# Kernel tuning notes

Hardware: AMD Instinct MI355X
Metric: run time of the kernel (lower is better)

Reference implementation:

```python
import jax, jax.numpy as jnp
import numpy as np

N = 50000   # nodes
E = 800000  # edges
B = 64      # graphs in batch
IN = 128    # in_features
HID = 64    # hidden_channels
H = 4       # head_count
C = 10      # out_classes
NEG = 0.2   # leaky relu negative slope
EPS = 1e-5  # batchnorm eps (eval mode, running mean 0 / var 1)


def _gat(x, edge_index, W, a_src, a_dst, b):
    """PyG GATConv (add_self_loops=False, concat=True), eval mode (no dropout)."""
    Hh, F = a_src.shape
    xW = (x @ W).reshape(-1, Hh, F)                       # [N,H,F]
    src, dst = edge_index[0], edge_index[1]
    e = (jnp.einsum('nhf,hf->nh', xW, a_src)[src]
         + jnp.einsum('nhf,hf->nh', xW, a_dst)[dst])      # [E,H]
    e = jnp.where(e > 0, e, NEG * e)                      # leaky relu
    m = jax.ops.segment_max(e, dst, num_segments=N)       # per-dst max
    m = jnp.where(jnp.isfinite(m), m, 0.0)
    p = jnp.exp(e - m[dst])
    denom = jax.ops.segment_sum(p, dst, num_segments=N)
    alpha = p / jnp.maximum(denom[dst], 1e-16)            # edge softmax over dst
    out = jax.ops.segment_sum(alpha[:, :, None] * xW[src], dst, num_segments=N)
    return out.reshape(-1, Hh * F) + b


def _bn_relu(y, g, be):
    # BatchNorm1d in eval mode with running_mean=0, running_var=1, then ReLU
    return jax.nn.relu(g * y / jnp.sqrt(1.0 + EPS) + be)


def setup_inputs():
    key = jax.random.key(0)
    ks = jax.random.split(key, 24)
    s = lambda k, shape: (jax.random.normal(k, shape, jnp.float32) * 0.05)
    z = lambda shape: jnp.zeros(shape, jnp.float32)
    o = lambda shape: jnp.ones(shape, jnp.float32)
    return {
        'acc_flag': 0,
        'x': jax.random.normal(ks[0], (N, IN), jnp.float32),
        'edge_index': jax.random.randint(ks[1], (2, E), 0, N),
        'batch': jnp.sort(jax.random.randint(ks[2], (N,), 0, B)),
        # layer 1: GATConv(IN -> HID, heads=H, concat)
        'W1': s(ks[3], (IN, H * HID)), 'a_src1': s(ks[4], (H, HID)), 'a_dst1': s(ks[5], (H, HID)), 'b1': z((H * HID,)),
        # proj: GATConv(H*HID -> HID, heads=1) + BN
        'W2': s(ks[6], (H * HID, HID)), 'a_src2': s(ks[7], (1, HID)), 'a_dst2': s(ks[8], (1, HID)), 'b2': z((HID,)), 'g2': o((HID,)), 'be2': z((HID,)),
        # block 1
        'W3': s(ks[9], (HID, HID)), 'a_src3': s(ks[10], (1, HID)), 'a_dst3': s(ks[11], (1, HID)), 'b3': z((HID,)), 'g3': o((HID,)), 'be3': z((HID,)),
        # block 2
        'W4': s(ks[12], (HID, HID)), 'a_src4': s(ks[13], (1, HID)), 'a_dst4': s(ks[14], (1, HID)), 'b4': z((HID,)), 'g4': o((HID,)), 'be4': z((HID,)),
        # MLP head
        'Wh1': s(ks[15], (HID, 128)), 'bh1': z((128,)),
        'Wh2': s(ks[16], (128, C)), 'bh2': z((C,)),
    }


def reference(acc_flag, x, edge_index, batch,
              W1, a_src1, a_dst1, b1,
              W2, a_src2, a_dst2, b2, g2, be2,
              W3, a_src3, a_dst3, b3, g3, be3,
              W4, a_src4, a_dst4, b4, g4, be4,
              Wh1, bh1, Wh2, bh2):
    # hardware GAT layer + ReLU (relu applied twice in original -> idempotent)
    x1 = jax.nn.relu(_gat(x, edge_index, W1, a_src1, a_dst1, b1))   # [N, H*HID]
    # projection block: residual base is zeros (shape mismatch H*HID vs HID)
    h = _bn_relu(_gat(x1, edge_index, W2, a_src2, a_dst2, b2), g2, be2)
    # residual blocks (shapes match -> x + relu(bn(y)))
    h = h + _bn_relu(_gat(h, edge_index, W3, a_src3, a_dst3, b3), g3, be3)
    h = h + _bn_relu(_gat(h, edge_index, W4, a_src4, a_dst4, b4), g4, be4)
    # global mean pool over graphs
    pooled = jax.ops.segment_sum(h, batch, num_segments=B)
    cnt = jnp.maximum(jax.ops.segment_sum(jnp.ones((N,), h.dtype), batch, num_segments=B), 1.0)
    hp = pooled / cnt[:, None]                                      # [B, HID]
    # MLP head
    return jax.nn.relu(hp @ Wh1 + bh1) @ Wh2 + bh2                  # [B, C]
```

## Files before the change

kernel.cpp:

```cpp
#include <hip/hip_runtime.h>

#define N_NODES 50000
#define N_EDGES 800000
#define N_GRAPHS 64
#define NEG_SLOPE 0.2f
#define BN_RSQ 0.9999950000374997f
#define NB_SCAN ((N_NODES + 255) / 256)

typedef __bf16 bf16x8 __attribute__((ext_vector_type(8)));
typedef float floatx4 __attribute__((ext_vector_type(4)));

__device__ __forceinline__ float lrelu(float v) { return v > 0.0f ? v : NEG_SLOPE * v; }

__device__ __forceinline__ float b2f(unsigned short u) {
    return __uint_as_float(((unsigned int)u) << 16);
}
__device__ __forceinline__ unsigned short f2b(float f) {
    unsigned int u = __float_as_uint(f);
    return (unsigned short)((u + 0x7fffu + ((u >> 16) & 1u)) >> 16);
}
__device__ __forceinline__ float blo(unsigned int d) { return __uint_as_float(d << 16); }
__device__ __forceinline__ float bhi(unsigned int d) { return __uint_as_float(d & 0xffff0000u); }

__global__ void k_prep(const int* __restrict__ ei, int* __restrict__ deg,
                       const float* __restrict__ W1, const float* __restrict__ W2,
                       const float* __restrict__ W3, const float* __restrict__ W4,
                       unsigned short* __restrict__ Wt1, unsigned short* __restrict__ Wt2,
                       unsigned short* __restrict__ Wt3, unsigned short* __restrict__ Wt4) {
    int i = blockIdx.x * 256 + threadIdx.x;
    if (i < 32768) {
        int k = i >> 8, n = i & 255;
        Wt1[n * 128 + k] = f2b(W1[i]);
    } else if (i < 49152) {
        int j = i - 32768;
        int k = j >> 6, n = j & 63;
        Wt2[n * 256 + k] = f2b(W2[j]);
    } else if (i < 53248) {
        int j = i - 49152;
        int k = j >> 6, n = j & 63;
        Wt3[n * 64 + k] = f2b(W3[j]);
    } else if (i < 57344) {
        int j = i - 53248;
        int k = j >> 6, n = j & 63;
        Wt4[n * 64 + k] = f2b(W4[j]);
    }
    if (i < N_EDGES) atomicAdd(&deg[ei[N_EDGES + i]], 1);
}

__global__ __launch_bounds__(256) void k_offs(const int* __restrict__ deg, int* __restrict__ offs,
                                              int* __restrict__ total, const int* __restrict__ batch,
                                              int* __restrict__ bounds, int* __restrict__ bh) {
    __shared__ int lh[64];
    if (threadIdx.x < 64) lh[threadIdx.x] = 0;
    __syncthreads();
    if (blockIdx.x == 0 && threadIdx.x <= N_GRAPHS) {
        int g = threadIdx.x;
        int lo = 0, hi = N_NODES;
        while (lo < hi) {
            int mid = (lo + hi) >> 1;
            if (batch[mid] < g) lo = mid + 1; else hi = mid;
        }
        bounds[g] = lo;
    }
    int i = blockIdx.x * blockDim.x + threadIdx.x;
    int lane = threadIdx.x & 63;
    int v = (i < N_NODES) ? deg[i] : 0;
    int incl = v;
    for (int o = 1; o < 64; o <<= 1) {
        int t = __shfl_up(incl, o);
        if (lane >= o) incl += t;
    }
    int wtot = __shfl(incl, 63);
    int base = 0;
    if (lane == 0) base = atomicAdd(total, wtot);
    base = __shfl(base, 0);
    if (i < N_NODES) {
        offs[i] = base + incl - v;
        atomicAdd(&lh[63 - min(v, 63)], 1);
    }
    __syncthreads();
    if (threadIdx.x < 64) bh[blockIdx.x * 64 + threadIdx.x] = lh[threadIdx.x];
}

__global__ __launch_bounds__(256) void k_pscan(const int* __restrict__ bh, int* __restrict__ bb) {
    __shared__ int partial[4][64];
    __shared__ int bbase[64];
    const int tid = threadIdx.x;
    const int b = tid & 63, q = tid >> 6;
    const int per = (NB_SCAN + 3) / 4;
    const int k0 = q * per, k1 = min(k0 + per, NB_SCAN);
    int s = 0;
    for (int k = k0; k < k1; ++k) s += bh[k * 64 + b];
    partial[q][b] = s;
    __syncthreads();
    if (tid < 64) {
        int tot = partial[0][tid] + partial[1][tid] + partial[2][tid] + partial[3][tid];
        int incl = tot;
        for (int o = 1; o < 64; o <<= 1) {
            int t2 = __shfl_up(incl, o);
            if (tid >= o) incl += t2;
        }
        bbase[tid] = incl - tot;
    }
    __syncthreads();
    int run = bbase[b];
    for (int q2 = 0; q2 < q; ++q2) run += partial[q2][b];
    for (int k = k0; k < k1; ++k) {
        bb[k * 64 + b] = run;
        run += bh[k * 64 + b];
    }
}

__global__ __launch_bounds__(256) void k_fillperm(const int* __restrict__ ei,
                                                  const int* __restrict__ offs,
                                                  int* __restrict__ cur, int* __restrict__ csr_src,
                                                  const int* __restrict__ deg,
                                                  const int* __restrict__ bb,
                                                  int* __restrict__ perm) {
    __shared__ int lcnt[64];
    if (blockIdx.x < NB_SCAN) {
        if (threadIdx.x < 64) lcnt[threadIdx.x] = 0;
        __syncthreads();
        int i = blockIdx.x * 256 + threadIdx.x;
        if (i < N_NODES) {
            int b = 63 - min(deg[i], 63);
            int r = atomicAdd(&lcnt[b], 1);
            perm[bb[blockIdx.x * 64 + b] + r] = i;
        }
    }
    int e = blockIdx.x * 256 + threadIdx.x;
    if (e < N_EDGES) {
        int d = ei[N_EDGES + e];
        int pos = offs[d] + atomicAdd(&cur[d], 1);
        csr_src[pos] = ei[e];
    }
}

template <int K, int N, int HEADS, bool AF32>
__global__ __launch_bounds__(256) void k_mgemm(const void* __restrict__ Ap,
                                               const unsigned short* __restrict__ Bt,
                                               const float* __restrict__ asrc,
                                               const float* __restrict__ adst,
                                               unsigned short* __restrict__ out,
                                               float* __restrict__ es,
                                               float* __restrict__ ed, int rows) {
    constexpr int LDP = K + 8;
    __shared__ unsigned short As[64 * LDP];
    const int tid = threadIdx.x;
    const int r0 = blockIdx.x * 64;
    if (AF32) {
        const float* A = (const float*)Ap;
        for (int i = tid; i < 16 * K; i += 256) {
            int r = i / (K / 4), c4 = i % (K / 4);
            int row = r0 + r;
            float4 v = (row < rows) ? *(const float4*)&A[(size_t)row * K + c4 * 4]
                                    : make_float4(0.f, 0.f, 0.f, 0.f);
            ushort4 u;
            u.x = f2b(v.x); u.y = f2b(v.y); u.z = f2b(v.z); u.w = f2b(v.w);
            *(ushort4*)&As[r * LDP + c4 * 4] = u;
        }
    } else {
        const unsigned short* A = (const unsigned short*)Ap;
        for (int i = tid; i < 8 * K; i += 256) {
            int r = i / (K / 8), c8 = i % (K / 8);
            int row = r0 + r;
            uint4 v;
            if (row < rows) v = *(const uint4*)&A[(size_t)row * K + c8 * 8];
            else { v.x = v.y = v.z = v.w = 0; }
            *(uint4*)&As[r * LDP + c8 * 8] = v;
        }
    }
    __syncthreads();
    const int w = tid >> 6, lane = tid & 63;
    const int quad = lane >> 4, l16 = lane & 15;
    const int gr0 = r0 + w * 16 + quad * 4;
    bf16x8 afrag[K / 32];
#pragma unroll
    for (int kk = 0; kk < K / 32; ++kk)
        afrag[kk] = *(const bf16x8*)&As[(w * 16 + l16) * LDP + kk * 32 + quad * 8];
    float sacc[4] = {0.f, 0.f, 0.f, 0.f};
    float dacc[4] = {0.f, 0.f, 0.f, 0.f};
#pragma unroll 1
    for (int ct = 0; ct < N / 16; ++ct) {
        floatx4 acc = {0.f, 0.f, 0.f, 0.f};
#pragma unroll
        for (int kk = 0; kk < K / 32; ++kk) {
            const bf16x8 bfrag =
                *(const bf16x8*)&Bt[(size_t)(ct * 16 + l16) * K + kk * 32 + quad * 8];
            acc = __builtin_amdgcn_mfma_f32_16x16x32_bf16(afrag[kk], bfrag, acc, 0, 0, 0);
        }
        const int gc = ct * 16 + l16;
        const int hh = gc >> 6;
        const int f = gc & 63;
        const float as = asrc[hh * 64 + f];
        const float ad = adst[hh * 64 + f];
#pragma unroll
        for (int rg = 0; rg < 4; ++rg) {
            sacc[rg] = fmaf(acc[rg], as, sacc[rg]);
            dacc[rg] = fmaf(acc[rg], ad, dacc[rg]);
        }
#pragma unroll
        for (int rg = 0; rg < 4; ++rg) {
            int gr = gr0 + rg;
            if (gr < rows) out[(size_t)gr * N + gc] = f2b(acc[rg]);
        }
        if ((ct & 3) == 3) {
#pragma unroll
            for (int rg = 0; rg < 4; ++rg) {
                float s = sacc[rg], d = dacc[rg];
                for (int o = 1; o < 16; o <<= 1) {
                    s += __shfl_xor(s, o);
                    d += __shfl_xor(d, o);
                }
                if (l16 == 0) {
                    int gr = gr0 + rg;
                    if (gr < rows) {
                        es[(size_t)gr * HEADS + hh] = s;
                        ed[(size_t)gr * HEADS + hh] = d;
                    }
                }
                sacc[rg] = 0.f;
                dacc[rg] = 0.f;
            }
        }
    }
}

__global__ __launch_bounds__(256) void k_gat1f(
    const unsigned short* __restrict__ xW, const float* __restrict__ es, const float* __restrict__ ed,
    const int* __restrict__ offs, const int* __restrict__ deg, const int* __restrict__ csr,
    const int* __restrict__ perm, const float* __restrict__ bias,
    const unsigned short* __restrict__ Bt2, const float* __restrict__ as2,
    const float* __restrict__ ad2, unsigned short* __restrict__ outW,
    float* __restrict__ es2o, float* __restrict__ ed2o) {
    __shared__ float ps[4][4 * 68];
    __shared__ int sbuf[4][64];
    __shared__ unsigned short As2[16 * 264];
    __shared__ int nbuf[16];
    __shared__ float sds[4][16], sdd[4][16];
    const int wv = threadIdx.x >> 6;
    const int lane = threadIdx.x & 63;
    const int grp = lane >> 4, t = lane & 15;
    const int h = t >> 2;
    const int r = wv * 4 + grp;
    const int pidx = blockIdx.x * 16 + r;
    const int n = perm[pidx];
    const int off = offs[n];
    const int dg = deg[n];
    const float4 edv = *(const float4*)&ed[n * 4];
    const int cb = t * 16;

    float acc[16];
#pragma unroll
    for (int k = 0; k < 16; ++k) acc[k] = 0.f;
    float dsum = 0.f;

    for (int base = 0; base < dg; base += 16) {
        const int idx = base + t;
        int s_l = 0;
        float p0 = 0.f, p1 = 0.f, p2 = 0.f, p3 = 0.f;
        if (idx < dg) {
            s_l = csr[off + idx];
            const float4 ev = *(const float4*)&es[s_l * 4];
            p0 = __expf(lrelu(ev.x + edv.x));
            p1 = __expf(lrelu(ev.y + edv.y));
            p2 = __expf(lrelu(ev.z + edv.z));
            p3 = __expf(lrelu(ev.w + edv.w));
        }
        *(float4*)&ps[wv][grp * 68 + t * 4] = make_float4(p0, p1, p2, p3);
        sbuf[wv][grp * 16 + t] = s_l;
        const int cnt = min(16, dg - base);
        const int cntR = (cnt + 3) & ~3;
        for (int j = 0; j < cntR; j += 4) {
            const float pa = ps[wv][grp * 68 + (j + 0) * 4 + h];
            const float pb = ps[wv][grp * 68 + (j + 1) * 4 + h];
            const float pc = ps[wv][grp * 68 + (j + 2) * 4 + h];
            const float pd = ps[wv][grp * 68 + (j + 3) * 4 + h];
            const int sa = sbuf[wv][grp * 16 + j + 0];
            const int sb = sbuf[wv][grp * 16 + j + 1];
            const int sc = sbuf[wv][grp * 16 + j + 2];
            const int sd = sbuf[wv][grp * 16 + j + 3];
            const uint4 a0 = *(const uint4*)&xW[(size_t)sa * 256 + cb];
            const uint4 a1 = *(const uint4*)&xW[(size_t)sa * 256 + cb + 8];
            const uint4 b0 = *(const uint4*)&xW[(size_t)sb * 256 + cb];
            const uint4 b1 = *(const uint4*)&xW[(size_t)sb * 256 + cb + 8];
            const uint4 c0 = *(const uint4*)&xW[(size_t)sc * 256 + cb];
            const uint4 c1 = *(const uint4*)&xW[(size_t)sc * 256 + cb + 8];
            const uint4 d0 = *(const uint4*)&xW[(size_t)sd * 256 + cb];
            const uint4 d1 = *(const uint4*)&xW[(size_t)sd * 256 + cb + 8];
            dsum += (pa + pb) + (pc + pd);
            acc[0]  = fmaf(pa, blo(a0.x), acc[0]);
            acc[1]  = fmaf(pa, bhi(a0.x), acc[1]);
            acc[2]  = fmaf(pa, blo(a0.y), acc[2]);
            acc[3]  = fmaf(pa, bhi(a0.y), acc[3]);
            acc[4]  = fmaf(pa, blo(a0.z), acc[4]);
            acc[5]  = fmaf(pa, bhi(a0.z), acc[5]);
            acc[6]  = fmaf(pa, blo(a0.w), acc[6]);
            acc[7]  = fmaf(pa, bhi(a0.w), acc[7]);
            acc[8]  = fmaf(pa, blo(a1.x), acc[8]);
            acc[9]  = fmaf(pa, bhi(a1.x), acc[9]);
            acc[10] = fmaf(pa, blo(a1.y), acc[10]);
            acc[11] = fmaf(pa, bhi(a1.y), acc[11]);
            acc[12] = fmaf(pa, blo(a1.z), acc[12]);
            acc[13] = fmaf(pa, bhi(a1.z), acc[13]);
            acc[14] = fmaf(pa, blo(a1.w), acc[14]);
            acc[15] = fmaf(pa, bhi(a1.w), acc[15]);
            acc[0]  = fmaf(pb, blo(b0.x), acc[0]);
            acc[1]  = fmaf(pb, bhi(b0.x), acc[1]);
            acc[2]  = fmaf(pb, blo(b0.y), acc[2]);
            acc[3]  = fmaf(pb, bhi(b0.y), acc[3]);
            acc[4]  = fmaf(pb, blo(b0.z), acc[4]);
            acc[5]  = fmaf(pb, bhi(b0.z), acc[5]);
            acc[6]  = fmaf(pb, blo(b0.w), acc[6]);
            acc[7]  = fmaf(pb, bhi(b0.w), acc[7]);
            acc[8]  = fmaf(pb, blo(b1.x), acc[8]);
            acc[9]  = fmaf(pb, bhi(b1.x), acc[9]);
            acc[10] = fmaf(pb, blo(b1.y), acc[10]);
            acc[11] = fmaf(pb, bhi(b1.y), acc[11]);
            acc[12] = fmaf(pb, blo(b1.z), acc[12]);
            acc[13] = fmaf(pb, bhi(b1.z), acc[13]);
            acc[14] = fmaf(pb, blo(b1.w), acc[14]);
            acc[15] = fmaf(pb, bhi(b1.w), acc[15]);
            acc[0]  = fmaf(pc, blo(c0.x), acc[0]);
            acc[1]  = fmaf(pc, bhi(c0.x), acc[1]);
            acc[2]  = fmaf(pc, blo(c0.y), acc[2]);
            acc[3]  = fmaf(pc, bhi(c0.y), acc[3]);
            acc[4]  = fmaf(pc, blo(c0.z), acc[4]);
            acc[5]  = fmaf(pc, bhi(c0.z), acc[5]);
            acc[6]  = fmaf(pc, blo(c0.w), acc[6]);
            acc[7]  = fmaf(pc, bhi(c0.w), acc[7]);
            acc[8]  = fmaf(pc, blo(c1.x), acc[8]);
            acc[9]  = fmaf(pc, bhi(c1.x), acc[9]);
            acc[10] = fmaf(pc, blo(c1.y), acc[10]);
            acc[11] = fmaf(pc, bhi(c1.y), acc[11]);
            acc[12] = fmaf(pc, blo(c1.z), acc[12]);
            acc[13] = fmaf(pc, bhi(c1.z), acc[13]);
            acc[14] = fmaf(pc, blo(c1.w), acc[14]);
            acc[15] = fmaf(pc, bhi(c1.w), acc[15]);
            acc[0]  = fmaf(pd, blo(d0.x), acc[0]);
            acc[1]  = fmaf(pd, bhi(d0.x), acc[1]);
            acc[2]  = fmaf(pd, blo(d0.y), acc[2]);
            acc[3]  = fmaf(pd, bhi(d0.y), acc[3]);
            acc[4]  = fmaf(pd, blo(d0.z), acc[4]);
            acc[5]  = fmaf(pd, bhi(d0.z), acc[5]);
            acc[6]  = fmaf(pd, blo(d0.w), acc[6]);
            acc[7]  = fmaf(pd, bhi(d0.w), acc[7]);
            acc[8]  = fmaf(pd, blo(d1.x), acc[8]);
            acc[9]  = fmaf(pd, bhi(d1.x), acc[9]);
            acc[10] = fmaf(pd, blo(d1.y), acc[10]);
            acc[11] = fmaf(pd, bhi(d1.y), acc[11]);
            acc[12] = fmaf(pd, blo(d1.z), acc[12]);
            acc[13] = fmaf(pd, bhi(d1.z), acc[13]);
            acc[14] = fmaf(pd, blo(d1.w), acc[14]);
            acc[15] = fmaf(pd, bhi(d1.w), acc[15]);
        }
    }
    const float inv = 1.0f / fmaxf(dsum, 1e-16f);
#pragma unroll
    for (int k4 = 0; k4 < 16; k4 += 4) {
        const int c = cb + k4;
        const float4 bv = *(const float4*)&bias[c];
        ushort4 o4;
        o4.x = f2b(fmaxf(fmaf(acc[k4 + 0], inv, bv.x), 0.f));
        o4.y = f2b(fmaxf(fmaf(acc[k4 + 1], inv, bv.y), 0.f));
        o4.z = f2b(fmaxf(fmaf(acc[k4 + 2], inv, bv.z), 0.f));
        o4.w = f2b(fmaxf(fmaf(acc[k4 + 3], inv, bv.w), 0.f));
        *(ushort4*)&As2[r * 264 + c] = o4;
    }
    if (t == 0) nbuf[r] = n;
    __syncthreads();

    {
        const int gc = wv * 16 + t;
        floatx4 c2 = {0.f, 0.f, 0.f, 0.f};
#pragma unroll
        for (int kk = 0; kk < 8; ++kk) {
            const bf16x8 af = *(const bf16x8*)&As2[t * 264 + kk * 32 + grp * 8];
            const bf16x8 bf = *(const bf16x8*)&Bt2[(size_t)gc * 256 + kk * 32 + grp * 8];
            c2 = __builtin_amdgcn_mfma_f32_16x16x32_bf16(af, bf, c2, 0, 0, 0);
        }
        const float a_s = as2[gc];
        const float a_d = ad2[gc];
        float srg[4], drg[4];
#pragma unroll
        for (int rg = 0; rg < 4; ++rg) {
            srg[rg] = c2[rg] * a_s;
            drg[rg] = c2[rg] * a_d;
            const int row = grp * 4 + rg;
            outW[(size_t)nbuf[row] * 64 + gc] = f2b(c2[rg]);
        }
#pragma unroll
        for (int rg = 0; rg < 4; ++rg) {
            for (int o = 1; o < 16; o <<= 1) {
                srg[rg] += __shfl_xor(srg[rg], o);
                drg[rg] += __shfl_xor(drg[rg], o);
            }
        }
        if (t == 0) {
#pragma unroll
            for (int rg = 0; rg < 4; ++rg) {
                sds[wv][grp * 4 + rg] = srg[rg];
                sdd[wv][grp * 4 + rg] = drg[rg];
            }
        }
    }
    __syncthreads();
    if (threadIdx.x < 16) {
        const int rr = threadIdx.x;
        es2o[nbuf[rr]] = sds[0][rr] + sds[1][rr] + sds[2][rr] + sds[3][rr];
        ed2o[nbuf[rr]] = sdd[0][rr] + sdd[1][rr] + sdd[2][rr] + sdd[3][rr];
    }
}

template <bool RES>
__global__ __launch_bounds__(256) void k_gatLG(
    const unsigned short* __restrict__ xW, const float* __restrict__ es, const float* __restrict__ ed,
    const int* __restrict__ offs, const int* __restrict__ deg, const int* __restrict__ csr,
    const int* __restrict__ perm, const float* __restrict__ bias, const float* __restrict__ gam,
    const float* __restrict__ bet, float* __restrict__ hglob,
    const unsigned short* __restrict__ Btn, const float* __restrict__ asn,
    const float* __restrict__ adn, unsigned short* __restrict__ outW,
    float* __restrict__ esn, float* __restrict__ edn_o) {
    __shared__ float ps[4][64];
    __shared__ int sbuf[4][64];
    __shared__ unsigned short As2[32 * 72];
    __shared__ int nbuf[32];
    __shared__ float sds[2][32], sdd[2][32];
    const int wv = threadIdx.x >> 6;
    const int lane = threadIdx.x & 63;
    const int g8 = lane >> 3, t8 = lane & 7;
    const int row1 = wv * 8 + g8;
    const int pbase = blockIdx.x * 32;
    const int pidx = pbase + row1;
    const bool valid = pidx < N_NODES;
    const int n = perm[valid ? pidx : 0];
    const int off = offs[n];
    const int dg = valid ? deg[n] : 0;
    const float edn = valid ? ed[n] : 0.f;
    const int cb = t8 * 8;

    float acc[8];
#pragma unroll
    for (int k = 0; k < 8; ++k) acc[k] = 0.f;
    float dsum = 0.f;

    for (int base = 0; base < dg; base += 8) {
        const int idx = base + t8;
        int s_l = 0;
        float p_l = 0.f;
        if (idx < dg) {
            s_l = csr[off + idx];
            p_l = __expf(lrelu(es[s_l] + edn));
        }
        ps[wv][g8 * 8 + t8] = p_l;
        sbuf[wv][g8 * 8 + t8] = s_l;
        float pp[8];
        int ss[8];
#pragma unroll
        for (int q = 0; q < 8; ++q) {
            pp[q] = ps[wv][g8 * 8 + q];
            ss[q] = sbuf[wv][g8 * 8 + q];
        }
        uint4 u[8];
#pragma unroll
        for (int q = 0; q < 8; ++q) u[q] = *(const uint4*)&xW[(size_t)ss[q] * 64 + cb];
#pragma unroll
        for (int q = 0; q < 8; ++q) {
            dsum += pp[q];
            acc[0] = fmaf(pp[q], blo(u[q].x), acc[0]);
            acc[1] = fmaf(pp[q], bhi(u[q].x), acc[1]);
            acc[2] = fmaf(pp[q], blo(u[q].y), acc[2]);
            acc[3] = fmaf(pp[q], bhi(u[q].y), acc[3]);
            acc[4] = fmaf(pp[q], blo(u[q].z), acc[4]);
            acc[5] = fmaf(pp[q], bhi(u[q].z), acc[5]);
            acc[6] = fmaf(pp[q], blo(u[q].w), acc[6]);
            acc[7] = fmaf(pp[q], bhi(u[q].w), acc[7]);
        }
    }
    const float inv = 1.0f / fmaxf(dsum, 1e-16f);
    float hn[8];
#pragma unroll
    for (int k = 0; k < 8; ++k) {
        const int c = cb + k;
        const float y = fmaf(acc[k], inv, bias[c]);
        const float z = fmaxf(fmaf(gam[c] * y, BN_RSQ, bet[c]), 0.f);
        hn[k] = (RES && valid) ? hglob[(size_t)n * 64 + c] + z : z;
    }
    if (valid) {
        *(float4*)&hglob[(size_t)n * 64 + cb] = make_float4(hn[0], hn[1], hn[2], hn[3]);
        *(float4*)&hglob[(size_t)n * 64 + cb + 4] = make_float4(hn[4], hn[5], hn[6], hn[7]);
    }
    ushort4 u0, u1;
    u0.x = f2b(hn[0]); u0.y = f2b(hn[1]); u0.z = f2b(hn[2]); u0.w = f2b(hn[3]);
    u1.x = f2b(hn[4]); u1.y = f2b(hn[5]); u1.z = f2b(hn[6]); u1.w = f2b(hn[7]);
    if (!valid) { u0.x = u0.y = u0.z = u0.w = 0; u1.x = u1.y = u1.z = u1.w = 0; }
    *(ushort4*)&As2[row1 * 72 + cb] = u0;
    *(ushort4*)&As2[row1 * 72 + cb + 4] = u1;
    if (t8 == 0) nbuf[row1] = n;
    __syncthreads();

    {
        const int quad = lane >> 4, l16 = lane & 15;
        const int rs = wv >> 1;
        float sacc[4] = {0.f, 0.f, 0.f, 0.f};
        float dacc[4] = {0.f, 0.f, 0.f, 0.f};
#pragma unroll
        for (int ci = 0; ci < 2; ++ci) {
            const int ct = (wv & 1) * 2 + ci;
            const int gc = ct * 16 + l16;
            floatx4 c2 = {0.f, 0.f, 0.f, 0.f};
#pragma unroll
            for (int kk = 0; kk < 2; ++kk) {
                const bf16x8 af = *(const bf16x8*)&As2[(rs * 16 + l16) * 72 + kk * 32 + quad * 8];
                const bf16x8 bf = *(const bf16x8*)&Btn[(size_t)gc * 64 + kk * 32 + quad * 8];
                c2 = __builtin_amdgcn_mfma_f32_16x16x32_bf16(af, bf, c2, 0, 0, 0);
            }
            const float a_s = asn[gc];
            const float a_d = adn[gc];
#pragma unroll
            for (int rg = 0; rg < 4; ++rg) {
                sacc[rg] = fmaf(c2[rg], a_s, sacc[rg]);
                dacc[rg] = fmaf(c2[rg], a_d, dacc[rg]);
                const int row = rs * 16 + quad * 4 + rg;
                if (pbase + row < N_NODES) outW[(size_t)nbuf[row] * 64 + gc] = f2b(c2[rg]);
            }
        }
#pragma unroll
        for (int rg = 0; rg < 4; ++rg) {
            for (int o = 1; o < 16; o <<= 1) {
                sacc[rg] += __shfl_xor(sacc[rg], o);
                dacc[rg] += __shfl_xor(dacc[rg], o);
            }
        }
        if (l16 == 0) {
#pragma unroll
            for (int rg = 0; rg < 4; ++rg) {
                sds[wv & 1][rs * 16 + quad * 4 + rg] = sacc[rg];
                sdd[wv & 1][rs * 16 + quad * 4 + rg] = dacc[rg];
            }
        }
    }
    __syncthreads();
    if (threadIdx.x < 32) {
        const int rr = threadIdx.x;
        if (pbase + rr < N_NODES) {
            esn[nbuf[rr]] = sds[0][rr] + sds[1][rr];
            edn_o[nbuf[rr]] = sdd[0][rr] + sdd[1][rr];
        }
    }
}

__global__ __launch_bounds__(256) void k_gatF(
    const unsigned short* __restrict__ xW, const float* __restrict__ es, const float* __restrict__ ed,
    const int* __restrict__ offs, const int* __restrict__ deg, const int* __restrict__ csr,
    const int* __restrict__ perm, const float* __restrict__ bias, const float* __restrict__ gam,
    const float* __restrict__ bet, float* __restrict__ h) {
    __shared__ float ps[4][64];
    __shared__ int sbuf[4][64];
    const int wv = threadIdx.x >> 6;
    const int lane = threadIdx.x & 63;
    const int grp = lane >> 3, t = lane & 7;
    const int pidx = blockIdx.x * 32 + wv * 8 + grp;
    if (pidx >= N_NODES) return;
    const int n = perm[pidx];
    const int off = offs[n];
    const int dg = deg[n];
    const float edn = ed[n];
    const int cb = t * 8;

    float acc[8];
#pragma unroll
    for (int k = 0; k < 8; ++k) acc[k] = 0.f;
    float dsum = 0.f;

    for (int base = 0; base < dg; base += 8) {
        const int idx = base + t;
        int s_l = 0;
        float p_l = 0.f;
        if (idx < dg) {
            s_l = csr[off + idx];
            p_l = __expf(lrelu(es[s_l] + edn));
        }
        ps[wv][grp * 8 + t] = p_l;
        sbuf[wv][grp * 8 + t] = s_l;
        float pp[8];
        int ss[8];
#pragma unroll
        for (int q = 0; q < 8; ++q) {
            pp[q] = ps[wv][grp * 8 + q];
            ss[q] = sbuf[wv][grp * 8 + q];
        }
        uint4 u[8];
#pragma unroll
        for (int q = 0; q < 8; ++q) u[q] = *(const uint4*)&xW[(size_t)ss[q] * 64 + cb];
#pragma unroll
        for (int q = 0; q < 8; ++q) {
            dsum += pp[q];
            acc[0] = fmaf(pp[q], blo(u[q].x), acc[0]);
            acc[1] = fmaf(pp[q], bhi(u[q].x), acc[1]);
            acc[2] = fmaf(pp[q], blo(u[q].y), acc[2]);
            acc[3] = fmaf(pp[q], bhi(u[q].y), acc[3]);
            acc[4] = fmaf(pp[q], blo(u[q].z), acc[4]);
            acc[5] = fmaf(pp[q], bhi(u[q].z), acc[5]);
            acc[6] = fmaf(pp[q], blo(u[q].w), acc[6]);
            acc[7] = fmaf(pp[q], bhi(u[q].w), acc[7]);
        }
    }
    const float inv = 1.0f / fmaxf(dsum, 1e-16f);
    float hn[8];
#pragma unroll
    for (int k = 0; k < 8; ++k) {
        const int c = cb + k;
        const float y = fmaf(acc[k], inv, bias[c]);
        const float z = fmaxf(fmaf(gam[c] * y, BN_RSQ, bet[c]), 0.f);
        hn[k] = h[(size_t)n * 64 + c] + z;
    }
    *(float4*)&h[(size_t)n * 64 + cb] = make_float4(hn[0], hn[1], hn[2], hn[3]);
    *(float4*)&h[(size_t)n * 64 + cb + 4] = make_float4(hn[4], hn[5], hn[6], hn[7]);
}

__global__ __launch_bounds__(256) void k_pool2(const float* __restrict__ h,
                                               const int* __restrict__ bounds,
                                               float* __restrict__ hp) {
    __shared__ float part[4][64];
    const int g = blockIdx.x;
    const int lane = threadIdx.x & 63;
    const int wid = threadIdx.x >> 6;
    const int s = bounds[g], e = bounds[g + 1];
    float acc = 0.f;
    for (int n = s + wid; n < e; n += 4) acc += h[n * 64 + lane];
    part[wid][lane] = acc;
    __syncthreads();
    if (wid == 0) {
        float v = part[0][lane] + part[1][lane] + part[2][lane] + part[3][lane];
        hp[g * 64 + lane] = v / fmaxf((float)(e - s), 1.0f);
    }
}

__global__ __launch_bounds__(256) void k_head(const float* __restrict__ hpg,
                                              const float* __restrict__ Wh1,
                                              const float* __restrict__ bh1,
                                              const float* __restrict__ Wh2,
                                              const float* __restrict__ bh2,
                                              float* __restrict__ out) {
    __shared__ float hp[64 * 64];
    __shared__ float t1[64 * 128];
    const int tid = threadIdx.x;
    for (int i = tid; i < 64 * 64; i += 256) hp[i] = hpg[i];
    __syncthreads();
    for (int i = tid; i < 64 * 128; i += 256) {
        int g = i >> 7, j = i & 127;
        float s = bh1[j];
        for (int k = 0; k < 64; ++k) s = fmaf(hp[g * 64 + k], Wh1[k * 128 + j], s);
        t1[i] = fmaxf(s, 0.f);
    }
    __syncthreads();
    for (int i = tid; i < 640; i += 256) {
        int g = i / 10, j = i - g * 10;
        float s = bh2[j];
        for (int k = 0; k < 128; ++k) s = fmaf(t1[g * 128 + k], Wh2[k * 10 + j], s);
        out[i] = s;
    }
}

extern "C" void kernel_launch(void* const* d_in, const int* in_sizes, int n_in,
                              void* d_out, int out_size, void* d_ws, size_t ws_size,
                              hipStream_t stream) {
    const float* x = (const float*)d_in[1];
    const int* ei = (const int*)d_in[2];
    const int* batch = (const int*)d_in[3];
    const float* W1 = (const float*)d_in[4];
    const float* a_src1 = (const float*)d_in[5];
    const float* a_dst1 = (const float*)d_in[6];
    const float* b1 = (const float*)d_in[7];
    const float* W2 = (const float*)d_in[8];
    const float* a_src2 = (const float*)d_in[9];
    const float* a_dst2 = (const float*)d_in[10];
    const float* b2 = (const float*)d_in[11];
    const float* g2 = (const float*)d_in[12];
    const float* be2 = (const float*)d_in[13];
    const float* W3 = (const float*)d_in[14];
    const float* a_src3 = (const float*)d_in[15];
    const float* a_dst3 = (const float*)d_in[16];
    const float* b3 = (const float*)d_in[17];
    const float* g3 = (const float*)d_in[18];
    const float* be3 = (const float*)d_in[19];
    const float* W4 = (const float*)d_in[20];
    const float* a_src4 = (const float*)d_in[21];
    const float* a_dst4 = (const float*)d_in[22];
    const float* b4 = (const float*)d_in[23];
    const float* g4 = (const float*)d_in[24];
    const float* be4 = (const float*)d_in[25];
    const float* Wh1 = (const float*)d_in[26];
    const float* bh1 = (const float*)d_in[27];
    const float* Wh2 = (const float*)d_in[28];
    const float* bh2 = (const float*)d_in[29];
    float* out = (float*)d_out;

    char* p = (char*)d_ws;
    auto alloc = [&](size_t bytes) {
        void* r = (void*)p;
        p += (bytes + 255) & ~(size_t)255;
        return r;
    };
    unsigned short* bufA1 = (unsigned short*)alloc((size_t)N_NODES * 256 * 2);
    unsigned short* bufB = (unsigned short*)alloc((size_t)N_NODES * 64 * 2);
    unsigned short* bufC = (unsigned short*)alloc((size_t)N_NODES * 64 * 2);
    unsigned short* bufD = (unsigned short*)alloc((size_t)N_NODES * 64 * 2);
    float* h = (float*)alloc((size_t)N_NODES * 64 * 4);
    float* es1 = (float*)alloc((size_t)N_NODES * 4 * 4);
    float* ed1 = (float*)alloc((size_t)N_NODES * 4 * 4);
    float* es2 = (float*)alloc((size_t)N_NODES * 4);
    float* ed2 = (float*)alloc((size_t)N_NODES * 4);
    float* es3 = (float*)alloc((size_t)N_NODES * 4);
    float* ed3 = (float*)alloc((size_t)N_NODES * 4);
    float* es4 = (float*)alloc((size_t)N_NODES * 4);
    float* ed4 = (float*)alloc((size_t)N_NODES * 4);
    int* offs = (int*)alloc((size_t)N_NODES * 4);
    int* csr = (int*)alloc((size_t)N_EDGES * 4);
    int* perm = (int*)alloc((size_t)N_NODES * 4);
    int* bounds = (int*)alloc((size_t)(N_GRAPHS + 1) * 4);
    int* bh_hist = (int*)alloc((size_t)NB_SCAN * 64 * 4);
    int* bb = (int*)alloc((size_t)NB_SCAN * 64 * 4);
    float* hpool = (float*)alloc((size_t)N_GRAPHS * 64 * 4);
    unsigned short* Wt1 = (unsigned short*)alloc((size_t)128 * 256 * 2);
    unsigned short* Wt2 = (unsigned short*)alloc((size_t)256 * 64 * 2);
    unsigned short* Wt3 = (unsigned short*)alloc((size_t)64 * 64 * 2);
    unsigned short* Wt4 = (unsigned short*)alloc((size_t)64 * 64 * 2);
    char* z0 = p;
    int* deg = (int*)alloc((size_t)N_NODES * 4);
    int* cur = (int*)alloc((size_t)N_NODES * 4);
    int* total = (int*)alloc(256);
    size_t zbytes = (size_t)(p - z0);
    hipMemsetAsync(z0, 0, zbytes, stream);

    const int edgeBlocks = (N_EDGES + 255) / 256;
    const int mgemmBlocks = (N_NODES + 63) / 64;
    const int gat1Blocks = (N_NODES + 15) / 16;
    const int gatLBlocks = (N_NODES + 31) / 32;

    k_prep<<<edgeBlocks, 256, 0, stream>>>(ei, deg, W1, W2, W3, W4, Wt1, Wt2, Wt3, Wt4);

    k_offs<<<NB_SCAN, 256, 0, stream>>>(deg, offs, total, batch, bounds, bh_hist);
    k_pscan<<<1, 256, 0, stream>>>(bh_hist, bb);
    k_fillperm<<<edgeBlocks, 256, 0, stream>>>(ei, offs, cur, csr, deg, bb, perm);

    k_mgemm<128, 256, 4, true><<<mgemmBlocks, 256, 0, stream>>>(x, Wt1, a_src1, a_dst1,
                                                                bufA1, es1, ed1, N_NODES);
    k_gat1f<<<gat1Blocks, 256, 0, stream>>>(bufA1, es1, ed1, offs, deg, csr, perm, b1,
                                            Wt2, a_src2, a_dst2, bufB, es2, ed2);

    k_gatLG<false><<<gatLBlocks, 256, 0, stream>>>(bufB, es2, ed2, offs, deg, csr, perm,
                                                   b2, g2, be2, h, Wt3, a_src3, a_dst3,
                                                   bufC, es3, ed3);
    k_gatLG<true><<<gatLBlocks, 256, 0, stream>>>(bufC, es3, ed3, offs, deg, csr, perm,
                                                  b3, g3, be3, h, Wt4, a_src4, a_dst4,
                                                  bufD, es4, ed4);
    k_gatF<<<gatLBlocks, 256, 0, stream>>>(bufD, es4, ed4, offs, deg, csr, perm, b4, g4, be4, h);

    k_pool2<<<N_GRAPHS, 256, 0, stream>>>(h, bounds, hpool);
    k_head<<<1, 256, 0, stream>>>(hpool, Wh1, bh1, Wh2, bh2, out);
}
```

Measured before the change: 511.8 us.

## Make fused next-layer projection per-wave, removing block barriers

The fused GAT kernels now have each wave compute its own rows' next-layer projection with transposed MFMA operands (weights as A, node rows as B). Shared-memory staging is per wave, so both __syncthreads barriers and the cross-wave partial-sum arrays go away. Outputs are written as ushort4 vectors instead of scalars. In exchange only 4 or 8 of the 16 MFMA columns carry real rows, so MFMA work is partly wasted, and each wave reloads the full weight matrix.

```diff
diff --git a/kernel.cpp b/kernel.cpp
--- a/kernel.cpp
+++ b/kernel.cpp
@@ -235,15 +235,12 @@
     float* __restrict__ es2o, float* __restrict__ ed2o) {
     __shared__ float ps[4][4 * 68];
     __shared__ int sbuf[4][64];
-    __shared__ unsigned short As2[16 * 264];
-    __shared__ int nbuf[16];
-    __shared__ float sds[4][16], sdd[4][16];
+    __shared__ unsigned short As2[4][4 * 264];
     const int wv = threadIdx.x >> 6;
     const int lane = threadIdx.x & 63;
     const int grp = lane >> 4, t = lane & 15;
     const int h = t >> 2;
-    const int r = wv * 4 + grp;
-    const int pidx = blockIdx.x * 16 + r;
+    const int pidx = blockIdx.x * 16 + wv * 4 + grp;
     const int n = perm[pidx];
     const int off = offs[n];
     const int dg = deg[n];
@@ -365,50 +362,34 @@
         o4.y = f2b(fmaxf(fmaf(acc[k4 + 1], inv, bv.y), 0.f));
         o4.z = f2b(fmaxf(fmaf(acc[k4 + 2], inv, bv.z), 0.f));
         o4.w = f2b(fmaxf(fmaf(acc[k4 + 3], inv, bv.w), 0.f));
-        *(ushort4*)&As2[r * 264 + c] = o4;
-    }
-    if (t == 0) nbuf[r] = n;
-    __syncthreads();
-
-    {
-        const int gc = wv * 16 + t;
+        *(ushort4*)&As2[wv][grp * 264 + c] = o4;
+    }
+    const int nl = __shfl(n, (t & 3) * 16);
+    float sred = 0.f, dred = 0.f;
+#pragma unroll
+    for (int ft = 0; ft < 4; ++ft) {
         floatx4 c2 = {0.f, 0.f, 0.f, 0.f};
 #pragma unroll
         for (int kk = 0; kk < 8; ++kk) {
-            const bf16x8 af = *(const bf16x8*)&As2[t * 264 + kk * 32 + grp * 8];
-            const bf16x8 bf = *(const bf16x8*)&Bt2[(size_t)gc * 256 + kk * 32 + grp * 8];
-            c2 = __builtin_amdgcn_mfma_f32_16x16x32_bf16(af, bf, c2, 0, 0, 0);
-        }
-        const float a_s = as2[gc];
-        const float a_d = ad2[gc];
-        float srg[4], drg[4];
-#pragma unroll
-        for (int rg = 0; rg < 4; ++rg) {
-            srg[rg] = c2[rg] * a_s;
-            drg[rg] = c2[rg] * a_d;
-            const int row = grp * 4 + rg;
-            outW[(size_t)nbuf[row] * 64 + gc] = f2b(c2[rg]);
-        }
-#pragma unroll
-        for (int rg = 0; rg < 4; ++rg) {
-            for (int o = 1; o < 16; o <<= 1) {
-                srg[rg] += __shfl_xor(srg[rg], o);
-                drg[rg] += __shfl_xor(drg[rg], o);
-            }
-        }
-        if (t == 0) {
-#pragma unroll
-            for (int rg = 0; rg < 4; ++rg) {
-                sds[wv][grp * 4 + rg] = srg[rg];
-                sdd[wv][grp * 4 + rg] = drg[rg];
-            }
-        }
-    }
-    __syncthreads();
-    if (threadIdx.x < 16) {
-        const int rr = threadIdx.x;
-        es2o[nbuf[rr]] = sds[0][rr] + sds[1][rr] + sds[2][rr] + sds[3][rr];
-        ed2o[nbuf[rr]] = sdd[0][rr] + sdd[1][rr] + sdd[2][rr] + sdd[3][rr];
+            const bf16x8 aw = *(const bf16x8*)&Bt2[(size_t)(ft * 16 + t) * 256 + kk * 32 + grp * 8];
+            const bf16x8 bx = *(const bf16x8*)&As2[wv][(t & 3) * 264 + kk * 32 + grp * 8];
+            c2 = __builtin_amdgcn_mfma_f32_16x16x32_bf16(aw, bx, c2, 0, 0, 0);
+        }
+        const float4 av = *(const float4*)&as2[ft * 16 + grp * 4];
+        const float4 dv = *(const float4*)&ad2[ft * 16 + grp * 4];
+        sred += c2[0] * av.x + c2[1] * av.y + c2[2] * av.z + c2[3] * av.w;
+        dred += c2[0] * dv.x + c2[1] * dv.y + c2[2] * dv.z + c2[3] * dv.w;
+        if (t < 4) {
+            ushort4 o;
+            o.x = f2b(c2[0]); o.y = f2b(c2[1]); o.z = f2b(c2[2]); o.w = f2b(c2[3]);
+            *(ushort4*)&outW[(size_t)nl * 64 + ft * 16 + grp * 4] = o;
+        }
+    }
+    sred += __shfl_xor(sred, 16); sred += __shfl_xor(sred, 32);
+    dred += __shfl_xor(dred, 16); dred += __shfl_xor(dred, 32);
+    if (grp == 0 && t < 4) {
+        es2o[nl] = sred;
+        ed2o[nl] = dred;
     }
 }
 
@@ -423,15 +404,13 @@
     float* __restrict__ esn, float* __restrict__ edn_o) {
     __shared__ float ps[4][64];
     __shared__ int sbuf[4][64];
-    __shared__ unsigned short As2[32 * 72];
-    __shared__ int nbuf[32];
-    __shared__ float sds[2][32], sdd[2][32];
+    __shared__ unsigned short As2[4][8 * 72];
     const int wv = threadIdx.x >> 6;
     const int lane = threadIdx.x & 63;
     const int g8 = lane >> 3, t8 = lane & 7;
-    const int row1 = wv * 8 + g8;
     const int pbase = blockIdx.x * 32;
-    const int pidx = pbase + row1;
+    if (pbase + wv * 8 >= N_NODES) return;
+    const int pidx = pbase + wv * 8 + g8;
     const bool valid = pidx < N_NODES;
     const int n = perm[valid ? pidx : 0];
     const int off = offs[n];
@@ -493,60 +472,36 @@
     ushort4 u0, u1;
     u0.x = f2b(hn[0]); u0.y = f2b(hn[1]); u0.z = f2b(hn[2]); u0.w = f2b(hn[3]);
     u1.x = f2b(hn[4]); u1.y = f2b(hn[5]); u1.z = f2b(hn[6]); u1.w = f2b(hn[7]);
-    if (!valid) { u0.x = u0.y = u0.z = u0.w = 0; u1.x = u1.y = u1.z = u1.w = 0; }
-    *(ushort4*)&As2[row1 * 72 + cb] = u0;
-    *(ushort4*)&As2[row1 * 72 + cb + 4] = u1;
-    if (t8 == 0) nbuf[row1] = n;
-    __syncthreads();
-
-    {
-        const int quad = lane >> 4, l16 = lane & 15;
-        const int rs = wv >> 1;
-        float sacc[4] = {0.f, 0.f, 0.f, 0.f};
-        float dacc[4] = {0.f, 0.f, 0.f, 0.f};
-#pragma unroll
-        for (int ci = 0; ci < 2; ++ci) {
-            const int ct = (wv & 1) * 2 + ci;
-            const int gc = ct * 16 + l16;
-            floatx4 c2 = {0.f, 0.f, 0.f, 0.f};
-#pragma unroll
-            for (int kk = 0; kk < 2; ++kk) {
-                const bf16x8 af = *(const bf16x8*)&As2[(rs * 16 + l16) * 72 + kk * 32 + quad * 8];
-                const bf16x8 bf = *(const bf16x8*)&Btn[(size_t)gc * 64 + kk * 32 + quad * 8];
-                c2 = __builtin_amdgcn_mfma_f32_16x16x32_bf16(af, bf, c2, 0, 0, 0);
-            }
-            const float a_s = asn[gc];
-            const float a_d = adn[gc];
-#pragma unroll
-            for (int rg = 0; rg < 4; ++rg) {
-                sacc[rg] = fmaf(c2[rg], a_s, sacc[rg]);
-                dacc[rg] = fmaf(c2[rg], a_d, dacc[rg]);
-                const int row = rs * 16 + quad * 4 + rg;
-                if (pbase + row < N_NODES) outW[(size_t)nbuf[row] * 64 + gc] = f2b(c2[rg]);
-            }
-        }
-#pragma unroll
-        for (int rg = 0; rg < 4; ++rg) {
-            for (int o = 1; o < 16; o <<= 1) {
-                sacc[rg] += __shfl_xor(sacc[rg], o);
-                dacc[rg] += __shfl_xor(dacc[rg], o);
-            }
-        }
-        if (l16 == 0) {
-#pragma unroll
-            for (int rg = 0; rg < 4; ++rg) {
-                sds[wv & 1][rs * 16 + quad * 4 + rg] = sacc[rg];
-                sdd[wv & 1][rs * 16 + quad * 4 + rg] = dacc[rg];
-            }
-        }
-    }
-    __syncthreads();
-    if (threadIdx.x < 32) {
-        const int rr = threadIdx.x;
-        if (pbase + rr < N_NODES) {
-            esn[nbuf[rr]] = sds[0][rr] + sds[1][rr];
-            edn_o[nbuf[rr]] = sdd[0][rr] + sdd[1][rr];
-        }
+    *(ushort4*)&As2[wv][g8 * 72 + cb] = u0;
+    *(ushort4*)&As2[wv][g8 * 72 + cb + 4] = u1;
+    const int quad = lane >> 4, l16 = lane & 15;
+    const int ncol = __shfl(n, (l16 & 7) * 8);
+    const bool vcol = (pbase + wv * 8 + (l16 & 7)) < N_NODES;
+    float sred = 0.f, dred = 0.f;
+#pragma unroll
+    for (int ft = 0; ft < 4; ++ft) {
+        floatx4 c2 = {0.f, 0.f, 0.f, 0.f};
+#pragma unroll
+        for (int kk = 0; kk < 2; ++kk) {
+            const bf16x8 aw = *(const bf16x8*)&Btn[(size_t)(ft * 16 + l16) * 64 + kk * 32 + quad * 8];
+            const bf16x8 bx = *(const bf16x8*)&As2[wv][(l16 & 7) * 72 + kk * 32 + quad * 8];
+            c2 = __builtin_amdgcn_mfma_f32_16x16x32_bf16(aw, bx, c2, 0, 0, 0);
+        }
+        const float4 av = *(const float4*)&asn[ft * 16 + quad * 4];
+        const float4 dv = *(const float4*)&adn[ft * 16 + quad * 4];
+        sred += c2[0] * av.x + c2[1] * av.y + c2[2] * av.z + c2[3] * av.w;
+        dred += c2[0] * dv.x + c2[1] * dv.y + c2[2] * dv.z + c2[3] * dv.w;
+        if (l16 < 8 && vcol) {
+            ushort4 o;
+            o.x = f2b(c2[0]); o.y = f2b(c2[1]); o.z = f2b(c2[2]); o.w = f2b(c2[3]);
+            *(ushort4*)&outW[(size_t)ncol * 64 + ft * 16 + quad * 4] = o;
+        }
+    }
+    sred += __shfl_xor(sred, 16); sred += __shfl_xor(sred, 32);
+    dred += __shfl_xor(dred, 16); dred += __shfl_xor(dred, 32);
+    if (quad == 0 && l16 < 8 && vcol) {
+        esn[ncol] = sred;
+        edn_o[ncol] = dred;
     }
 }
 
```

New measurement: 544.6 us. 6.4% more time.
